# Kernel tuning notes

Hardware: AMD Instinct MI355X
Metric: run time of the kernel (lower is better)

The kernel has to match this reference:

```python
import jax, jax.numpy as jnp
import numpy as np

EPS = 1e-7  # K.epsilon()

def squash(v, axis=-1):
    sn = jnp.sum(jnp.square(v), axis=axis, keepdims=True)
    scale = sn / (1.0 + sn) / jnp.sqrt(sn + EPS)
    return scale * v

def setup_inputs() -> dict:
    key = jax.random.key(0)
    k1, k2, k3 = jax.random.split(key, 3)
    B, In, Din = 32, 2048, 8
    N, Dout, C = 64, 16, 32
    x = jax.random.normal(k1, (B, In, Din), dtype=jnp.float32)
    W = jax.random.normal(k2, (N, C, Dout, Din), dtype=jnp.float32) * 0.1
    B_bias = jax.random.normal(k3, (N, Dout), dtype=jnp.float32) * 0.1
    return {"x": x, "W": W, "B_bias": B_bias}

def reference(x, W, B_bias):
    routings = 3
    N, C, Dout, Din = W.shape
    In = x.shape[1]
    # repeat channel weights to cover all input capsules: [N, In, Dout, Din]
    W2 = jnp.repeat(W, In // C, axis=1)
    # vote vectors: inputs_hat[b,n,i,d] = sum_k x[b,i,k] * W2[n,i,d,k]
    inputs_hat = jnp.einsum('bik,nidk->bnid', x, W2)  # [B, N, In, Dout]
    b = jnp.zeros(inputs_hat.shape[:3], dtype=inputs_hat.dtype)  # [B, N, In]
    outputs = None
    for i in range(routings):
        c = jax.nn.softmax(b, axis=1)  # softmax over num_capsule axis
        s = jnp.einsum('bni,bnid->bnd', c, inputs_hat) + B_bias
        outputs = squash(s)
        if i < routings - 1:
            b = b + jnp.einsum('bnd,bnid->bni', outputs, inputs_hat)
    return outputs
```

## Files before the change

### kernel.cpp

```cpp
#include <hip/hip_runtime.h>
#include <math.h>

constexpr int B_    = 32;
constexpr int In_   = 2048;
constexpr int Din_  = 8;
constexpr int N_    = 64;
constexpr int Dout_ = 16;
constexpr int C_    = 32;
constexpr int ICP   = 64;
constexpr float EPS = 1e-7f;

__global__ __launch_bounds__(256) void caps_v0(
    const float* __restrict__ x, const float* __restrict__ W,
    const float* __restrict__ bias, float* __restrict__ v0)
{
    const int b = blockIdx.x >> 3, j = blockIdx.x & 7;
    const int t = threadIdx.x;

    __shared__ float xbar[C_][Din_];

    {
        const int c = t >> 3, k = t & 7;
        const float* xp = x + (size_t)b * In_ * Din_ + (size_t)c * ICP * Din_ + k;
        float acc = 0.f;
        #pragma unroll 8
        for (int i = 0; i < ICP; ++i) acc += xp[i * Din_];
        xbar[c][k] = acc * (1.f / 64.f);
    }
    __syncthreads();

    {
        const int nl = t >> 5, lane32 = t & 31;
        const int d = lane32 >> 1, h = lane32 & 1;
        const int n = j * 8 + nl;

        float a = 0.f;
        #pragma unroll
        for (int cc = 0; cc < 16; ++cc) {
            const int c2 = cc * 2 + h;
            const float4* wp = (const float4*)(W + (((size_t)n * C_ + c2) * Dout_ + d) * Din_);
            const float4 w0 = wp[0], w1 = wp[1];
            a += w0.x * xbar[c2][0] + w0.y * xbar[c2][1] + w0.z * xbar[c2][2] + w0.w * xbar[c2][3]
               + w1.x * xbar[c2][4] + w1.y * xbar[c2][5] + w1.z * xbar[c2][6] + w1.w * xbar[c2][7];
        }
        a += __shfl_xor(a, 1);
        a += bias[n * Dout_ + d];

        float sn = a * a;
        sn += __shfl_xor(sn, 2);
        sn += __shfl_xor(sn, 4);
        sn += __shfl_xor(sn, 8);
        sn += __shfl_xor(sn, 16);
        const float sc = sn / (1.f + sn) / sqrtf(sn + EPS);
        if (h == 0) v0[(size_t)b * 1024 + n * Dout_ + d] = a * sc;
    }
}

__global__ __launch_bounds__(256) void caps_route(
    const float* __restrict__ x, const float* __restrict__ W,
    const float* __restrict__ v_src, float* __restrict__ s_out)
{
    const int b = blockIdx.x >> 5;
    const int c = blockIdx.x & 31;
    const int t = threadIdx.x;
    const int w = t >> 6, l = t & 63;
    const int n4 = t >> 2, q4 = t & 3;

    __shared__ float Us[N_][8];
    __shared__ float xs[ICP][8];
    __shared__ float lg[ICP][68];
    __shared__ float ps[4][ICP];
    __shared__ float inv_s[ICP];
    __shared__ float ys[4][N_][8];

    {
        const float4 vv = *(const float4*)(v_src + ((size_t)b * 64 + n4) * 16 + q4 * 4);
        const float vd[4] = {vv.x, vv.y, vv.z, vv.w};
        float pU[8] = {0, 0, 0, 0, 0, 0, 0, 0};
        #pragma unroll
        for (int dd = 0; dd < 4; ++dd) {
            const int d = q4 * 4 + dd;
            const float4* wp = (const float4*)(W + (((size_t)n4 * 32 + c) * 16 + d) * 8);
            const float4 w0 = wp[0], w1 = wp[1];
            const float v_ = vd[dd];
            pU[0] += v_ * w0.x; pU[1] += v_ * w0.y; pU[2] += v_ * w0.z; pU[3] += v_ * w0.w;
            pU[4] += v_ * w1.x; pU[5] += v_ * w1.y; pU[6] += v_ * w1.z; pU[7] += v_ * w1.w;
        }
        #pragma unroll
        for (int k = 0; k < 8; ++k) {
            pU[k] += __shfl_xor(pU[k], 1);
            pU[k] += __shfl_xor(pU[k], 2);
        }
        float2 u2; u2.x = pU[2 * q4]; u2.y = pU[2 * q4 + 1];
        *(float2*)&Us[n4][2 * q4] = u2;
    }

    float xr[8];
    {
        const float4* xp = (const float4*)(x + ((size_t)b * In_ + c * ICP + l) * 8);
        const float4 x0 = xp[0], x1 = xp[1];
        xr[0] = x0.x; xr[1] = x0.y; xr[2] = x0.z; xr[3] = x0.w;
        xr[4] = x1.x; xr[5] = x1.y; xr[6] = x1.z; xr[7] = x1.w;
        if (w == 0) { *(float4*)&xs[l][0] = x0; *(float4*)&xs[l][4] = x1; }
    }
    __syncthreads();

    {
        float e[16];
        float ssum = 0.f;
        #pragma unroll
        for (int nn = 0; nn < 16; ++nn) {
            const int n = w * 16 + nn;
            const float4 u0 = *(const float4*)&Us[n][0];
            const float4 u1 = *(const float4*)&Us[n][4];
            const float a = u0.x * xr[0] + u0.y * xr[1] + u0.z * xr[2] + u0.w * xr[3]
                          + u1.x * xr[4] + u1.y * xr[5] + u1.z * xr[6] + u1.w * xr[7];
            const float ee = __expf(a);
            e[nn] = ee; ssum += ee;
        }
        #pragma unroll
        for (int qq = 0; qq < 4; ++qq) {
            float4 o;
            o.x = e[qq * 4 + 0]; o.y = e[qq * 4 + 1]; o.z = e[qq * 4 + 2]; o.w = e[qq * 4 + 3];
            *(float4*)&lg[l][w * 16 + qq * 4] = o;
        }
        ps[w][l] = ssum;
    }
    __syncthreads();

    if (t < 64) inv_s[t] = 1.f / (ps[0][t] + ps[1][t] + ps[2][t] + ps[3][t]);
    __syncthreads();

    {
        const int nq = l >> 2, kq = l & 3;
        float y[8] = {0, 0, 0, 0, 0, 0, 0, 0};
        #pragma unroll
        for (int ii = 0; ii < 16; ++ii) {
            const int i = w * 16 + ii;
            const float4 cw = *(const float4*)&lg[i][nq * 4];
            const float iv = inv_s[i];
            const float2 x2 = *(const float2*)&xs[i][kq * 2];
            const float c0 = cw.x * iv, c1 = cw.y * iv, c2 = cw.z * iv, c3 = cw.w * iv;
            y[0] += c0 * x2.x; y[1] += c0 * x2.y;
            y[2] += c1 * x2.x; y[3] += c1 * x2.y;
            y[4] += c2 * x2.x; y[5] += c2 * x2.y;
            y[6] += c3 * x2.x; y[7] += c3 * x2.y;
        }
        #pragma unroll
        for (int jj = 0; jj < 4; ++jj) {
            float2 o; o.x = y[2 * jj]; o.y = y[2 * jj + 1];
            *(float2*)&ys[w][nq * 4 + jj][kq * 2] = o;
        }
    }
    __syncthreads();

    {
        float yn[8];
        #pragma unroll
        for (int k = 0; k < 8; ++k)
            yn[k] = ys[0][n4][k] + ys[1][n4][k] + ys[2][n4][k] + ys[3][n4][k];
        float4 o;
        float* op = (float*)&o;
        #pragma unroll
        for (int dd = 0; dd < 4; ++dd) {
            const int d = q4 * 4 + dd;
            const float4* wp = (const float4*)(W + (((size_t)n4 * 32 + c) * 16 + d) * 8);
            const float4 w0 = wp[0], w1 = wp[1];
            op[dd] = w0.x * yn[0] + w0.y * yn[1] + w0.z * yn[2] + w0.w * yn[3]
                   + w1.x * yn[4] + w1.y * yn[5] + w1.z * yn[6] + w1.w * yn[7];
        }
        *(float4*)(s_out + (((size_t)b * 32 + c) * 64 + n4) * 16 + q4 * 4) = o;
    }
}

__global__ __launch_bounds__(256) void caps_reduce(
    const float* __restrict__ s_src, const float* __restrict__ bias,
    const float* __restrict__ vadd, float* __restrict__ dst)
{
    const int b = blockIdx.x >> 3, j = blockIdx.x & 7;
    const int t = threadIdx.x;
    const int nl = t >> 5, lane32 = t & 31;
    const int d = lane32 >> 1, h = lane32 & 1;
    const int n = j * 8 + nl;

    float a = 0.f;
    #pragma unroll
    for (int cc = 0; cc < 16; ++cc) {
        const int c2 = cc * 2 + h;
        a += s_src[(((size_t)b * 32 + c2) * 64 + n) * 16 + d];
    }
    a += __shfl_xor(a, 1);
    a += bias[n * Dout_ + d];

    float sn = a * a;
    sn += __shfl_xor(sn, 2);
    sn += __shfl_xor(sn, 4);
    sn += __shfl_xor(sn, 8);
    sn += __shfl_xor(sn, 16);
    const float sc = sn / (1.f + sn) / sqrtf(sn + EPS);
    float val = a * sc;
    if (vadd) val += vadd[(size_t)b * 1024 + n * Dout_ + d];
    if (h == 0) dst[(size_t)b * 1024 + n * Dout_ + d] = val;
}

extern "C" void kernel_launch(void* const* d_in, const int* in_sizes, int n_in,
                              void* d_out, int out_size, void* d_ws, size_t ws_size,
                              hipStream_t stream) {
    const float* x    = (const float*)d_in[0];
    const float* W    = (const float*)d_in[1];
    const float* bias = (const float*)d_in[2];
    float* out = (float*)d_out;

    float* ws   = (float*)d_ws;
    float* s1   = ws;
    float* s2   = s1   + (size_t)B_ * C_ * N_ * Dout_;
    float* v0   = s2   + (size_t)B_ * C_ * N_ * Dout_;
    float* vsum = v0   + (size_t)B_ * N_ * Dout_;

    caps_v0    <<<256,  256, 0, stream>>>(x, W, bias, v0);
    caps_route <<<1024, 256, 0, stream>>>(x, W, v0, s1);
    caps_reduce<<<256,  256, 0, stream>>>(s1, bias, v0, vsum);
    caps_route <<<1024, 256, 0, stream>>>(x, W, vsum, s2);
    caps_reduce<<<256,  256, 0, stream>>>(s2, bias, nullptr, out);
}
```

Measured before the change: 90.38 us.

## Fuse routing pipeline into single persistent cooperative kernel with grid syncs

Merges the five separate launches (v0, two route passes, two reductions) into one cooperative kernel of 512 persistent blocks that synchronise with grid.sync between stages, each block processing two route tiles sequentially. Shared memory is unified into a struct reused across stages. This aims to remove per-launch overhead and inter-kernel gaps, at the cost of grid-wide barrier latency and lower concurrency per stage. A fallback to the multi-kernel path remains if occupancy is insufficient.

Result: slower. 92.55 us (+2.4%).

```diff
diff --git a/kernel.cpp b/kernel.cpp
--- a/kernel.cpp
+++ b/kernel.cpp
@@ -1,5 +1,8 @@
 #include <hip/hip_runtime.h>
+#include <hip/hip_cooperative_groups.h>
 #include <math.h>
+
+namespace cg = cooperative_groups;
 
 constexpr int B_    = 32;
 constexpr int In_   = 2048;
@@ -8,16 +11,26 @@
 constexpr int Dout_ = 16;
 constexpr int C_    = 32;
 constexpr int ICP   = 64;
+constexpr int GRID  = 512;
 constexpr float EPS = 1e-7f;
 
-__global__ __launch_bounds__(256) void caps_v0(
+struct Smem {
+    float Us[N_][8];
+    float xs[ICP][8];
+    float lg[ICP][68];
+    float ps[4][ICP];
+    float inv_s[ICP];
+    float ys[4][N_][8];
+};
+
+__device__ __forceinline__ void v0_body(
+    Smem* sm, int blk,
     const float* __restrict__ x, const float* __restrict__ W,
     const float* __restrict__ bias, float* __restrict__ v0)
 {
-    const int b = blockIdx.x >> 3, j = blockIdx.x & 7;
+    const int b = blk >> 3, j = blk & 7;
     const int t = threadIdx.x;
-
-    __shared__ float xbar[C_][Din_];
+    float (*xbar)[8] = (float(*)[8])(&sm->Us[0][0]);
 
     {
         const int c = t >> 3, k = t & 7;
@@ -56,22 +69,16 @@
     }
 }
 
-__global__ __launch_bounds__(256) void caps_route(
+__device__ __forceinline__ void route_body(
+    Smem* sm, int blk,
     const float* __restrict__ x, const float* __restrict__ W,
     const float* __restrict__ v_src, float* __restrict__ s_out)
 {
-    const int b = blockIdx.x >> 5;
-    const int c = blockIdx.x & 31;
+    const int b = blk >> 5;
+    const int c = blk & 31;
     const int t = threadIdx.x;
     const int w = t >> 6, l = t & 63;
     const int n4 = t >> 2, q4 = t & 3;
-
-    __shared__ float Us[N_][8];
-    __shared__ float xs[ICP][8];
-    __shared__ float lg[ICP][68];
-    __shared__ float ps[4][ICP];
-    __shared__ float inv_s[ICP];
-    __shared__ float ys[4][N_][8];
 
     {
         const float4 vv = *(const float4*)(v_src + ((size_t)b * 64 + n4) * 16 + q4 * 4);
@@ -92,7 +99,7 @@
             pU[k] += __shfl_xor(pU[k], 2);
         }
         float2 u2; u2.x = pU[2 * q4]; u2.y = pU[2 * q4 + 1];
-        *(float2*)&Us[n4][2 * q4] = u2;
+        *(float2*)&sm->Us[n4][2 * q4] = u2;
     }
 
     float xr[8];
@@ -101,7 +108,7 @@
         const float4 x0 = xp[0], x1 = xp[1];
         xr[0] = x0.x; xr[1] = x0.y; xr[2] = x0.z; xr[3] = x0.w;
         xr[4] = x1.x; xr[5] = x1.y; xr[6] = x1.z; xr[7] = x1.w;
-        if (w == 0) { *(float4*)&xs[l][0] = x0; *(float4*)&xs[l][4] = x1; }
+        if (w == 0) { *(float4*)&sm->xs[l][0] = x0; *(float4*)&sm->xs[l][4] = x1; }
     }
     __syncthreads();
 
@@ -111,8 +118,8 @@
         #pragma unroll
         for (int nn = 0; nn < 16; ++nn) {
             const int n = w * 16 + nn;
-            const float4 u0 = *(const float4*)&Us[n][0];
-            const float4 u1 = *(const float4*)&Us[n][4];
+            const float4 u0 = *(const float4*)&sm->Us[n][0];
+            const float4 u1 = *(const float4*)&sm->Us[n][4];
             const float a = u0.x * xr[0] + u0.y * xr[1] + u0.z * xr[2] + u0.w * xr[3]
                           + u1.x * xr[4] + u1.y * xr[5] + u1.z * xr[6] + u1.w * xr[7];
             const float ee = __expf(a);
@@ -122,13 +129,13 @@
         for (int qq = 0; qq < 4; ++qq) {
             float4 o;
             o.x = e[qq * 4 + 0]; o.y = e[qq * 4 + 1]; o.z = e[qq * 4 + 2]; o.w = e[qq * 4 + 3];
-            *(float4*)&lg[l][w * 16 + qq * 4] = o;
-        }
-        ps[w][l] = ssum;
-    }
-    __syncthreads();
-
-    if (t < 64) inv_s[t] = 1.f / (ps[0][t] + ps[1][t] + ps[2][t] + ps[3][t]);
+            *(float4*)&sm->lg[l][w * 16 + qq * 4] = o;
+        }
+        sm->ps[w][l] = ssum;
+    }
+    __syncthreads();
+
+    if (t < 64) sm->inv_s[t] = 1.f / (sm->ps[0][t] + sm->ps[1][t] + sm->ps[2][t] + sm->ps[3][t]);
     __syncthreads();
 
     {
@@ -137,9 +144,9 @@
         #pragma unroll
         for (int ii = 0; ii < 16; ++ii) {
             const int i = w * 16 + ii;
-            const float4 cw = *(const float4*)&lg[i][nq * 4];
-            const float iv = inv_s[i];
-            const float2 x2 = *(const float2*)&xs[i][kq * 2];
+            const float4 cw = *(const float4*)&sm->lg[i][nq * 4];
+            const float iv = sm->inv_s[i];
+            const float2 x2 = *(const float2*)&sm->xs[i][kq * 2];
             const float c0 = cw.x * iv, c1 = cw.y * iv, c2 = cw.z * iv, c3 = cw.w * iv;
             y[0] += c0 * x2.x; y[1] += c0 * x2.y;
             y[2] += c1 * x2.x; y[3] += c1 * x2.y;
@@ -149,7 +156,7 @@
         #pragma unroll
         for (int jj = 0; jj < 4; ++jj) {
             float2 o; o.x = y[2 * jj]; o.y = y[2 * jj + 1];
-            *(float2*)&ys[w][nq * 4 + jj][kq * 2] = o;
+            *(float2*)&sm->ys[w][nq * 4 + jj][kq * 2] = o;
         }
     }
     __syncthreads();
@@ -158,7 +165,7 @@
         float yn[8];
         #pragma unroll
         for (int k = 0; k < 8; ++k)
-            yn[k] = ys[0][n4][k] + ys[1][n4][k] + ys[2][n4][k] + ys[3][n4][k];
+            yn[k] = sm->ys[0][n4][k] + sm->ys[1][n4][k] + sm->ys[2][n4][k] + sm->ys[3][n4][k];
         float4 o;
         float* op = (float*)&o;
         #pragma unroll
@@ -173,11 +180,11 @@
     }
 }
 
-__global__ __launch_bounds__(256) void caps_reduce(
-    const float* __restrict__ s_src, const float* __restrict__ bias,
+__device__ __forceinline__ void reduce_body(
+    int blk, const float* __restrict__ s_src, const float* __restrict__ bias,
     const float* __restrict__ vadd, float* __restrict__ dst)
 {
-    const int b = blockIdx.x >> 3, j = blockIdx.x & 7;
+    const int b = blk >> 3, j = blk & 7;
     const int t = threadIdx.x;
     const int nl = t >> 5, lane32 = t & 31;
     const int d = lane32 >> 1, h = lane32 & 1;
@@ -203,6 +210,58 @@
     if (h == 0) dst[(size_t)b * 1024 + n * Dout_ + d] = val;
 }
 
+__global__ __launch_bounds__(256, 2) void caps_fused(
+    const float* __restrict__ x, const float* __restrict__ W,
+    const float* __restrict__ bias, float* __restrict__ out,
+    float* __restrict__ s1, float* __restrict__ s2,
+    float* __restrict__ v0, float* __restrict__ vsum)
+{
+    __shared__ Smem sm;
+    cg::grid_group grid = cg::this_grid();
+    const int blk = blockIdx.x;
+
+    if (blk < 256) v0_body(&sm, blk, x, W, bias, v0);
+    grid.sync();
+
+    route_body(&sm, blk, x, W, v0, s1);
+    __syncthreads();
+    route_body(&sm, blk + 512, x, W, v0, s1);
+    grid.sync();
+
+    if (blk < 256) reduce_body(blk, s1, bias, v0, vsum);
+    grid.sync();
+
+    route_body(&sm, blk, x, W, vsum, s2);
+    __syncthreads();
+    route_body(&sm, blk + 512, x, W, vsum, s2);
+    grid.sync();
+
+    if (blk < 256) reduce_body(blk, s2, bias, nullptr, out);
+}
+
+__global__ __launch_bounds__(256) void caps_v0_k(
+    const float* __restrict__ x, const float* __restrict__ W,
+    const float* __restrict__ bias, float* __restrict__ v0)
+{
+    __shared__ Smem sm;
+    v0_body(&sm, blockIdx.x, x, W, bias, v0);
+}
+
+__global__ __launch_bounds__(256) void caps_route_k(
+    const float* __restrict__ x, const float* __restrict__ W,
+    const float* __restrict__ v_src, float* __restrict__ s_out)
+{
+    __shared__ Smem sm;
+    route_body(&sm, blockIdx.x, x, W, v_src, s_out);
+}
+
+__global__ __launch_bounds__(256) void caps_reduce_k(
+    const float* __restrict__ s_src, const float* __restrict__ bias,
+    const float* __restrict__ vadd, float* __restrict__ dst)
+{
+    reduce_body(blockIdx.x, s_src, bias, vadd, dst);
+}
+
 extern "C" void kernel_launch(void* const* d_in, const int* in_sizes, int n_in,
                               void* d_out, int out_size, void* d_ws, size_t ws_size,
                               hipStream_t stream) {
@@ -217,9 +276,32 @@
     float* v0   = s2   + (size_t)B_ * C_ * N_ * Dout_;
     float* vsum = v0   + (size_t)B_ * N_ * Dout_;
 
-    caps_v0    <<<256,  256, 0, stream>>>(x, W, bias, v0);
-    caps_route <<<1024, 256, 0, stream>>>(x, W, v0, s1);
-    caps_reduce<<<256,  256, 0, stream>>>(s1, bias, v0, vsum);
-    caps_route <<<1024, 256, 0, stream>>>(x, W, vsum, s2);
-    caps_reduce<<<256,  256, 0, stream>>>(s2, bias, nullptr, out);
-}
+    static int use_coop = -1;
+    if (use_coop < 0) {
+        int dev = 0;
+        (void)hipGetDevice(&dev);
+        int occ = 0;
+        (void)hipOccupancyMaxActiveBlocksPerMultiprocessor(
+            &occ, (const void*)caps_fused, 256, 0);
+        int cus = 0;
+        (void)hipDeviceGetAttribute(&cus, hipDeviceAttributeMultiprocessorCount, dev);
+        use_coop = (occ > 0 && cus > 0 && (long)occ * (long)cus >= GRID) ? 1 : 0;
+    }
+
+    if (use_coop) {
+        void* args[] = {
+            (void*)&x, (void*)&W, (void*)&bias, (void*)&out,
+            (void*)&s1, (void*)&s2, (void*)&v0, (void*)&vsum
+        };
+        hipError_t e = hipLaunchCooperativeKernel((void*)caps_fused, dim3(GRID),
+                                                  dim3(256), args, 0, stream);
+        if (e == hipSuccess) return;
+        use_coop = 0;
+    }
+
+    caps_v0_k    <<<256,  256, 0, stream>>>(x, W, bias, v0);
+    caps_route_k <<<1024, 256, 0, stream>>>(x, W, v0, s1);
+    caps_reduce_k<<<256,  256, 0, stream>>>(s1, bias, v0, vsum);
+    caps_route_k <<<1024, 256, 0, stream>>>(x, W, vsum, s2);
+    caps_reduce_k<<<256,  256, 0, stream>>>(s2, bias, nullptr, out);
+}
```
